# Kernel optimization log

Hardware: AMD Instinct MI355X
Metric: run time of the kernel (lower is better)

## Reference

```python
import jax, jax.numpy as jnp
import numpy as np

POOL = 7            # pool_size
IMG_H, IMG_W = 432.0, 768.0   # hardcoded image size in cal_rois_ratio


def setup_inputs() -> dict:
    key = jax.random.key(0)
    k1, k2 = jax.random.split(key)
    feature_map = jax.random.normal(k1, (16, 27, 48, 512), dtype=jnp.float32)
    raw = jax.random.uniform(k2, (16, 100, 4), dtype=jnp.float32)
    # (cx, cy, w, h) in pixel coordinates of a 768x432 image
    cx = raw[..., 0] * IMG_W
    cy = raw[..., 1] * IMG_H
    w = raw[..., 2] * 300.0 + 8.0
    h = raw[..., 3] * 200.0 + 8.0
    nmses = jnp.stack([cx, cy, w, h], axis=-1)
    return {"feature_map": feature_map, "nmses": nmses}


def _crop_and_resize(feature_map, boxes, box_idx, crop):
    # Faithful tf.image.crop_and_resize (bilinear, extrapolation_value=0).
    B, H, W, C = feature_map.shape
    N = boxes.shape[0]
    t = jnp.arange(crop, dtype=feature_map.dtype)  # [P]
    y1, x1, y2, x2 = boxes[:, 0:1], boxes[:, 1:2], boxes[:, 2:3], boxes[:, 3:4]
    # sample coordinates in source feature-map space, [N, P]
    ys = y1 * (H - 1) + t[None, :] * (y2 - y1) * (H - 1) / (crop - 1)
    xs = x1 * (W - 1) + t[None, :] * (x2 - x1) * (W - 1) / (crop - 1)
    vy = (ys >= 0) & (ys <= H - 1)
    vx = (xs >= 0) & (xs <= W - 1)
    y0f = jnp.floor(ys)
    x0f = jnp.floor(xs)
    ly = ys - y0f  # lerp weights, [N, P]
    lx = xs - x0f
    y0 = jnp.clip(y0f.astype(jnp.int32), 0, H - 1)
    y1i = jnp.clip(y0 + 1, 0, H - 1)
    x0 = jnp.clip(x0f.astype(jnp.int32), 0, W - 1)
    x1i = jnp.clip(x0 + 1, 0, W - 1)
    b = box_idx[:, None, None]  # [N,1,1]
    # four bilinear corners, each [N, P, P, C]
    tl = feature_map[b, y0[:, :, None], x0[:, None, :]]
    tr = feature_map[b, y0[:, :, None], x1i[:, None, :]]
    bl = feature_map[b, y1i[:, :, None], x0[:, None, :]]
    br = feature_map[b, y1i[:, :, None], x1i[:, None, :]]
    lxg = lx[:, None, :, None]
    lyg = ly[:, :, None, None]
    top = tl + (tr - tl) * lxg
    bot = bl + (br - bl) * lxg
    out = top + (bot - top) * lyg
    mask = (vy[:, :, None] & vx[:, None, :])[..., None]
    return jnp.where(mask, out, jnp.zeros((), out.dtype))


def reference(feature_map, nmses):
    B, H, W, C = feature_map.shape
    R = nmses.shape[1]
    # cal_rois_ratio: (cx,cy,w,h) pixels -> normalized (y1,x1,y2,x2)
    x1 = (nmses[..., 0] - nmses[..., 2] / 2) / IMG_W
    x2 = (nmses[..., 0] + nmses[..., 2] / 2) / IMG_W
    y1 = (nmses[..., 1] - nmses[..., 3] / 2) / IMG_H
    y2 = (nmses[..., 1] + nmses[..., 3] / 2) / IMG_H
    boxes = jnp.stack([y1, x1, y2, x2], axis=-1).reshape(-1, 4)  # [B*R, 4]
    box_idx = jnp.repeat(jnp.arange(B), R)  # [B*R]
    rois = _crop_and_resize(feature_map, boxes, box_idx, POOL)  # [B*R, P, P, C]
    return rois.reshape(B, R, POOL, POOL, C)
```

## Files before the change

kernel.cpp:

```cpp
#include <hip/hip_runtime.h>

#define BB   16
#define RR   100
#define HH   27
#define WW   48
#define CC   512
#define PP   7

#define C4       (CC / 4)
#define ROW4     (WW * C4)
#define IMG4     (HH * ROW4)

#define TOTAL4   (BB * RR * PP * PP * C4)
#define NTHREADS (TOTAL4 / 2)
#define NBLOCKS  (NTHREADS / 256)
#define NXCD     8

typedef float vf4 __attribute__((ext_vector_type(4)));

__global__ __launch_bounds__(256) void roi_crop_resize_kernel(
    const float* __restrict__ fm,
    const float* __restrict__ nms,
    float* __restrict__ out)
{
    const int bid  = blockIdx.x;
    const int wgid = (bid % NXCD) * (NBLOCKS / NXCD) + bid / NXCD;

    const int idx  = wgid * 256 + threadIdx.x;
    const int c4   = idx & 63;
    const int cell = idx >> 6;

    const int px = cell % PP;
    int t        = cell / PP;
    const int py = t % PP;
    t           /= PP;

    const int ts = __builtin_amdgcn_readfirstlane(t);
    const int b  = ts / RR;

    const vf4 box = ((const vf4*)nms)[ts];
    const float cx = box.x, cy = box.y, w = box.z, h = box.w;

    const float x1 = (cx - w * 0.5f) / 768.0f;
    const float x2 = (cx + w * 0.5f) / 768.0f;
    const float y1 = (cy - h * 0.5f) / 432.0f;
    const float y2 = (cy + h * 0.5f) / 432.0f;

    const float ys = y1 * 26.0f + (float)py * (y2 - y1) * 26.0f / 6.0f;
    const float xs = x1 * 47.0f + (float)px * (x2 - x1) * 47.0f / 6.0f;

    const bool valid = (ys >= 0.0f) && (ys <= 26.0f) &&
                       (xs >= 0.0f) && (xs <= 47.0f);

    vf4 o0, o1;
    if (valid) {
        const float y0f = floorf(ys);
        const float x0f = floorf(xs);
        const float ly = ys - y0f;
        const float lx = xs - x0f;

        int y0 = (int)y0f; y0 = min(max(y0, 0), HH - 1);
        const int y1i = min(y0 + 1, HH - 1);
        int x0 = (int)x0f; x0 = min(max(x0, 0), WW - 1);
        const int x1i = min(x0 + 1, WW - 1);

        const vf4* img = ((const vf4*)fm) + (size_t)b * IMG4;
        const vf4* rT  = img + y0  * ROW4;
        const vf4* rB  = img + y1i * ROW4;

        const vf4 tl0 = rT[x0  * C4 + c4];
        const vf4 tr0 = rT[x1i * C4 + c4];
        const vf4 bl0 = rB[x0  * C4 + c4];
        const vf4 br0 = rB[x1i * C4 + c4];
        const vf4 tl1 = rT[x0  * C4 + c4 + 64];
        const vf4 tr1 = rT[x1i * C4 + c4 + 64];
        const vf4 bl1 = rB[x0  * C4 + c4 + 64];
        const vf4 br1 = rB[x1i * C4 + c4 + 64];

        const vf4 top0 = tl0 + (tr0 - tl0) * lx;
        const vf4 bot0 = bl0 + (br0 - bl0) * lx;
        o0 = top0 + (bot0 - top0) * ly;
        const vf4 top1 = tl1 + (tr1 - tl1) * lx;
        const vf4 bot1 = bl1 + (br1 - bl1) * lx;
        o1 = top1 + (bot1 - top1) * ly;
    } else {
        o0 = (vf4)(0.0f);
        o1 = (vf4)(0.0f);
    }

    vf4* op = ((vf4*)out) + (size_t)cell * C4 + c4;
    __builtin_nontemporal_store(o0, op);
    __builtin_nontemporal_store(o1, op + 64);
}

extern "C" void kernel_launch(void* const* d_in, const int* in_sizes, int n_in,
                              void* d_out, int out_size, void* d_ws, size_t ws_size,
                              hipStream_t stream)
{
    const float* fm  = (const float*)d_in[0];
    const float* nms = (const float*)d_in[1];
    float* out = (float*)d_out;

    roi_crop_resize_kernel<<<NBLOCKS, 256, 0, stream>>>(fm, nms, out);
}
```

Measured before the change: 37.58 us.

## Stage ROI source rows into LDS per box column before bilinear sampling

The kernel is restructured so each workgroup handles one (box, output column) pair, with seven waves covering the seven output rows. The workgroup first copies the vertical span of source rows and the two needed columns of the feature map into shared memory, then interpolates from LDS instead of issuing scattered global loads. The aim is to cut redundant global or L2 reads of corner pixels shared between neighbouring output rows. In exchange it adds a barrier, about 61KB of LDS per workgroup (which limits occupancy), and a bounded row buffer (YMAX) that relies on the box-height range of the inputs.

After: 58.29 us. +55.1%, slower.

```diff
diff --git a/kernel.cpp b/kernel.cpp
--- a/kernel.cpp
+++ b/kernel.cpp
@@ -7,38 +7,32 @@
 #define CC   512
 #define PP   7
 
-#define C4       (CC / 4)
-#define ROW4     (WW * C4)
-#define IMG4     (HH * ROW4)
+#define C4    (CC / 4)
+#define ROW4  (WW * C4)
+#define IMG4  (HH * ROW4)
 
-#define TOTAL4   (BB * RR * PP * PP * C4)
-#define NTHREADS (TOTAL4 / 2)
-#define NBLOCKS  (NTHREADS / 256)
-#define NXCD     8
+#define NBOX  (BB * RR)
+#define NBLK  (NBOX * PP)
+#define NXCD  8
+#define YMAX  15
 
 typedef float vf4 __attribute__((ext_vector_type(4)));
 
-__global__ __launch_bounds__(256) void roi_crop_resize_kernel(
+__global__ __launch_bounds__(448) void roi_stage_kernel(
     const float* __restrict__ fm,
     const float* __restrict__ nms,
     float* __restrict__ out)
 {
-    const int bid  = blockIdx.x;
-    const int wgid = (bid % NXCD) * (NBLOCKS / NXCD) + bid / NXCD;
+    __shared__ vf4 st[YMAX][2][C4];
 
-    const int idx  = wgid * 256 + threadIdx.x;
-    const int c4   = idx & 63;
-    const int cell = idx >> 6;
+    const int bid = blockIdx.x;
+    const int wg  = (bid % NXCD) * (NBLK / NXCD) + bid / NXCD;
 
-    const int px = cell % PP;
-    int t        = cell / PP;
-    const int py = t % PP;
-    t           /= PP;
+    const int px = wg % PP;
+    const int t  = wg / PP;
+    const int b  = t / RR;
 
-    const int ts = __builtin_amdgcn_readfirstlane(t);
-    const int b  = ts / RR;
-
-    const vf4 box = ((const vf4*)nms)[ts];
+    const vf4 box = ((const vf4*)nms)[t];
     const float cx = box.x, cy = box.y, w = box.z, h = box.w;
 
     const float x1 = (cx - w * 0.5f) / 768.0f;
@@ -46,36 +40,61 @@
     const float y1 = (cy - h * 0.5f) / 432.0f;
     const float y2 = (cy + h * 0.5f) / 432.0f;
 
-    const float ys = y1 * 26.0f + (float)py * (y2 - y1) * 26.0f / 6.0f;
     const float xs = x1 * 47.0f + (float)px * (x2 - x1) * 47.0f / 6.0f;
+    const bool  vx = (xs >= 0.0f) && (xs <= 47.0f);
 
-    const bool valid = (ys >= 0.0f) && (ys <= 26.0f) &&
-                       (xs >= 0.0f) && (xs <= 47.0f);
+    const int tid  = threadIdx.x;
+    const int lane = tid & 63;
+    const int wid  = tid >> 6;
+
+    const float x0f = floorf(xs);
+    const float lx  = xs - x0f;
+    int x0 = (int)x0f; x0 = min(max(x0, 0), WW - 1);
+    const int x1i   = min(x0 + 1, WW - 1);
+    const int xbase = min(x0, WW - 2);
+    const int sx0   = x0  - xbase;
+    const int sx1   = x1i - xbase;
+
+    const float ysA = y1 * 26.0f + 0.0f * (y2 - y1) * 26.0f / 6.0f;
+    const float ysB = y1 * 26.0f + 6.0f * (y2 - y1) * 26.0f / 6.0f;
+    int ylo = (int)floorf(ysA); ylo = min(max(ylo, 0), HH - 1);
+    int yhi = (int)floorf(ysB); yhi = min(max(yhi, 0), HH - 1);
+    yhi = min(yhi + 1, HH - 1);
+    const int yspan = yhi - ylo + 1;
+
+    if (vx) {
+        const vf4* src = ((const vf4*)fm) + (size_t)b * IMG4
+                         + (size_t)ylo * ROW4 + (size_t)xbase * C4;
+        const int n4 = yspan * 256;
+        vf4* dst = &st[0][0][0];
+        for (int i = tid; i < n4; i += 448) {
+            const int r = i >> 8;
+            const int j = i & 255;
+            dst[i] = src[(size_t)r * ROW4 + j];
+        }
+    }
+    __syncthreads();
+
+    const float ys = y1 * 26.0f + (float)wid * (y2 - y1) * 26.0f / 6.0f;
+    const bool  vy = (ys >= 0.0f) && (ys <= 26.0f);
 
     vf4 o0, o1;
-    if (valid) {
+    if (vx && vy) {
         const float y0f = floorf(ys);
-        const float x0f = floorf(xs);
-        const float ly = ys - y0f;
-        const float lx = xs - x0f;
+        const float ly  = ys - y0f;
+        int y0 = (int)y0f; y0 = min(max(y0, 0), HH - 1);
+        const int y1r = min(y0 + 1, HH - 1);
+        const int r0  = y0  - ylo;
+        const int r1  = y1r - ylo;
 
-        int y0 = (int)y0f; y0 = min(max(y0, 0), HH - 1);
-        const int y1i = min(y0 + 1, HH - 1);
-        int x0 = (int)x0f; x0 = min(max(x0, 0), WW - 1);
-        const int x1i = min(x0 + 1, WW - 1);
-
-        const vf4* img = ((const vf4*)fm) + (size_t)b * IMG4;
-        const vf4* rT  = img + y0  * ROW4;
-        const vf4* rB  = img + y1i * ROW4;
-
-        const vf4 tl0 = rT[x0  * C4 + c4];
-        const vf4 tr0 = rT[x1i * C4 + c4];
-        const vf4 bl0 = rB[x0  * C4 + c4];
-        const vf4 br0 = rB[x1i * C4 + c4];
-        const vf4 tl1 = rT[x0  * C4 + c4 + 64];
-        const vf4 tr1 = rT[x1i * C4 + c4 + 64];
-        const vf4 bl1 = rB[x0  * C4 + c4 + 64];
-        const vf4 br1 = rB[x1i * C4 + c4 + 64];
+        const vf4 tl0 = st[r0][sx0][lane];
+        const vf4 tr0 = st[r0][sx1][lane];
+        const vf4 bl0 = st[r1][sx0][lane];
+        const vf4 br0 = st[r1][sx1][lane];
+        const vf4 tl1 = st[r0][sx0][lane + 64];
+        const vf4 tr1 = st[r0][sx1][lane + 64];
+        const vf4 bl1 = st[r1][sx0][lane + 64];
+        const vf4 br1 = st[r1][sx1][lane + 64];
 
         const vf4 top0 = tl0 + (tr0 - tl0) * lx;
         const vf4 bot0 = bl0 + (br0 - bl0) * lx;
@@ -88,7 +107,8 @@
         o1 = (vf4)(0.0f);
     }
 
-    vf4* op = ((vf4*)out) + (size_t)cell * C4 + c4;
+    const int cell = t * (PP * PP) + wid * PP + px;
+    vf4* op = ((vf4*)out) + (size_t)cell * C4 + lane;
     __builtin_nontemporal_store(o0, op);
     __builtin_nontemporal_store(o1, op + 64);
 }
@@ -101,5 +121,5 @@
     const float* nms = (const float*)d_in[1];
     float* out = (float*)d_out;
 
-    roi_crop_resize_kernel<<<NBLOCKS, 256, 0, stream>>>(fm, nms, out);
+    roi_stage_kernel<<<NBLK, 448, 0, stream>>>(fm, nms, out);
 }
```
